# Performance work log

Hardware: AMD Instinct MI355X
Metric: run time of the kernel (lower is better)

The kernel has to match this reference:

```python
import jax, jax.numpy as jnp
import numpy as np

NUM_ROUTES, NUM_TIME, DIM, K, C = 100000, 2016, 256, 100, 5
BATCH = 262144


def _xavier(key, shape):
    fan_in, fan_out = shape[0], shape[1]
    lim = np.sqrt(6.0 / (fan_in + fan_out))
    return jax.random.uniform(key, shape, jnp.float32, -lim, lim)


def setup_inputs() -> dict:
    key = jax.random.key(0)
    ks = jax.random.split(key, 9)
    route_idx = jax.random.randint(ks[0], (BATCH,), 0, NUM_ROUTES)
    time_idx = jax.random.randint(ks[1], (BATCH,), 0, NUM_TIME)
    route_table = _xavier(ks[2], (NUM_ROUTES, DIM))
    time_table = _xavier(ks[3], (NUM_TIME, DIM))
    w = _xavier(ks[4], (DIM, K))
    mode_a = _xavier(ks[5], (DIM, C))
    mode_b = _xavier(ks[6], (DIM, C))
    mode_bias = jnp.zeros((C, C), jnp.float32)
    fc_lim = 1.0 / np.sqrt(C * C + K)
    fc_w = jax.random.uniform(ks[7], (C * C + K, 1), jnp.float32, -fc_lim, fc_lim)
    fc_b = jax.random.uniform(ks[8], (1,), jnp.float32, -fc_lim, fc_lim)
    return {
        "route_idx": route_idx, "time_idx": time_idx,
        "route_table": route_table, "time_table": time_table,
        "w": w, "mode_a": mode_a, "mode_b": mode_b,
        "mode_bias": mode_bias, "fc_w": fc_w, "fc_b": fc_b,
    }


def reference(route_idx, time_idx, route_table, time_table, w, mode_a, mode_b, mode_bias, fc_w, fc_b):
    r = route_table[route_idx]            # [B, D]
    t = time_table[time_idx]              # [B, D]
    gcp = jax.nn.relu((r * t) @ w)        # [B, K]
    # einsum('ni,nj->nij') then contracting i with mode_a and j with mode_b
    # equals outer product of the two small projections (exact same math):
    ra = r @ mode_a                       # [B, C]
    tb = t @ mode_b                       # [B, C]
    inter = jax.nn.sigmoid(ra[:, :, None] * tb[:, None, :] + mode_bias)  # [B, C, C]
    feats = jnp.concatenate([gcp, inter.reshape(inter.shape[0], -1)], axis=1)  # [B, K + C*C]
    out = feats @ fc_w + fc_b             # [B, 1]
    return jnp.squeeze(out, axis=-1)      # [B]
```

## Files before the change

### kernel.cpp

```cpp
#include <hip/hip_runtime.h>
#include <stdint.h>

#define BATCH   262144
#define NROUTES 100000
#define NTIME   2016
#define DIM     256
#define KOUT    100
#define NTILES  7

typedef __attribute__((ext_vector_type(2))) float f32x2;
typedef __attribute__((ext_vector_type(4))) float f32x4;

#define WS_WFRAG_BYTES ((size_t)(NTILES * 8 * 64 * 8))
#define WS_RA_OFF   (WS_WFRAG_BYTES)
#define WS_TB_OFF   (WS_RA_OFF + (size_t)NROUTES * 32)
#define WS_RT8_OFF  (WS_TB_OFF + (size_t)NTIME * 32)
#define WS_TT8_OFF  (WS_RT8_OFF + (size_t)NROUTES * 256)
#define WS_NEED     (WS_TT8_OFF + (size_t)NTIME * 256)

template<int CTRL>
static __device__ __forceinline__ float dpp_add(float x) {
  int s = __builtin_amdgcn_update_dpp(0, __builtin_bit_cast(int, x), CTRL, 0xF, 0xF, true);
  return x + __builtin_bit_cast(float, s);
}
static __device__ __forceinline__ float wave_sum63(float x) {
  x = dpp_add<0x111>(x);
  x = dpp_add<0x112>(x);
  x = dpp_add<0x114>(x);
  x = dpp_add<0x118>(x);
  x = dpp_add<0x142>(x);
  x = dpp_add<0x143>(x);
  return x;
}
static __device__ __forceinline__ float sum16_all(float x) {
  x = dpp_add<0x0B1>(x);
  x = dpp_add<0x04E>(x);
  x = dpp_add<0x124>(x);
  x = dpp_add<0x128>(x);
  return x;
}
static __device__ __forceinline__ float sigm(float z) {
  return __builtin_amdgcn_rcpf(1.0f + __expf(-z));
}

__global__ __launch_bounds__(256) void prep_kernel(
    const float* __restrict__ route_table,
    const float* __restrict__ time_table,
    const float* __restrict__ w,
    const float* __restrict__ mode_a,
    const float* __restrict__ mode_b,
    uint8_t* __restrict__ ws, int do8)
{
  const int b   = blockIdx.x;
  const int tid = threadIdx.x;

  if (b < 14) {
    const int u = b * 256 + tid;
    const int lane = u & 63;
    const int frag = u >> 6;
    const int ks = frag / NTILES;
    const int nt = frag % NTILES;
    const int n  = nt * 16 + (lane & 15);
    const int k0 = ks * 32 + (lane >> 4) * 8;
    float v[8];
    #pragma unroll
    for (int j = 0; j < 8; ++j)
      v[j] = (n < KOUT) ? w[(size_t)(k0 + j) * KOUT + n] : 0.0f;
    uint32_t d0 = 0, d1 = 0;
    d0 = __builtin_amdgcn_cvt_pk_fp8_f32(v[0], v[1], d0, false);
    d0 = __builtin_amdgcn_cvt_pk_fp8_f32(v[2], v[3], d0, true);
    d1 = __builtin_amdgcn_cvt_pk_fp8_f32(v[4], v[5], d1, false);
    d1 = __builtin_amdgcn_cvt_pk_fp8_f32(v[6], v[7], d1, true);
    ((uint2*)ws)[u] = make_uint2(d0, d1);
    return;
  }

  const float* tab; const float* proj; float* outp; uint8_t* out8; int base;
  if (b < 14 + 126) {
    tab = time_table;  proj = mode_b; outp = (float*)(ws + WS_TB_OFF);
    out8 = ws + WS_TT8_OFF; base = (b - 14) * 16;
  } else {
    tab = route_table; proj = mode_a; outp = (float*)(ws + WS_RA_OFF);
    out8 = ws + WS_RT8_OFF; base = (b - 140) * 16;
  }

  const int wave = tid >> 6, lane = tid & 63;
  float A[4][5];
  #pragma unroll
  for (int j = 0; j < 4; ++j)
    #pragma unroll
    for (int i = 0; i < 5; ++i)
      A[j][i] = proj[(4 * lane + j) * 5 + i];

  const int p0 = (lane >> 4) * 64 + ((lane >> 1) & 3) * 16 +
                 ((lane >> 3) & 1) * 8 + (lane & 1) * 4;

  const int row0 = base + wave * 4;
  float4 v[4];
  #pragma unroll
  for (int rr = 0; rr < 4; ++rr)
    v[rr] = *(const float4*)(tab + (size_t)(row0 + rr) * DIM + 4 * lane);

  #pragma unroll
  for (int rr = 0; rr < 4; ++rr) {
    const int row = row0 + rr;
    if (do8) {
      uint32_t u = 0;
      u = __builtin_amdgcn_cvt_pk_fp8_f32(8.f * v[rr].x, 8.f * v[rr].y, u, false);
      u = __builtin_amdgcn_cvt_pk_fp8_f32(8.f * v[rr].z, 8.f * v[rr].w, u, true);
      *(uint32_t*)(out8 + (size_t)row * 256 + p0) = u;
    }
    float p[5];
    #pragma unroll
    for (int i = 0; i < 5; ++i) {
      float s = v[rr].x * A[0][i] + v[rr].y * A[1][i] + v[rr].z * A[2][i] + v[rr].w * A[3][i];
      p[i] = wave_sum63(s);
    }
    if (lane == 63) {
      float* o = outp + (size_t)row * 8;
      *(f32x4*)o = (f32x4){p[0], p[1], p[2], p[3]};
      o[4] = p[4];
    }
  }
}

template<int TAB8>
__global__ __launch_bounds__(256, 4) void main_kernel(
    const int*   __restrict__ route_idx,
    const int*   __restrict__ time_idx,
    const float* __restrict__ route_table,
    const float* __restrict__ time_table,
    const float* __restrict__ mode_bias,
    const float* __restrict__ fc_w,
    const float* __restrict__ fc_b,
    const uint8_t* __restrict__ ws,
    float* __restrict__ out)
{
  __shared__ uint4 wlds[1792];
  const int tid  = threadIdx.x;
  const int wave = tid >> 6, lane = tid & 63;
  const int col  = lane & 15, quad = lane >> 4;
  const int m0   = blockIdx.x * 64 + wave * 16;
  const size_t ri = (size_t)route_idx[m0 + col];
  const size_t ti = (size_t)time_idx[m0 + col];

  uint4 rw[4], tw[4];
  if (TAB8) {
    const uint8_t* rb = ws + WS_RT8_OFF + ri * 256 + quad * 16;
    const uint8_t* tb = ws + WS_TT8_OFF + ti * 256 + quad * 16;
    #pragma unroll
    for (int i = 0; i < 4; ++i) {
      rw[i] = *(const uint4*)(rb + i * 64);
      tw[i] = *(const uint4*)(tb + i * 64);
    }
  }
  const float* rap = (const float*)(ws + WS_RA_OFF) + ri * 8;
  const float* tbp = (const float*)(ws + WS_TB_OFF) + ti * 8;
  f32x4 ra0 = *(const f32x4*)rap; float ra4 = rap[4];
  f32x4 tb0 = *(const f32x4*)tbp; float tb4 = tbp[4];

  {
    const uint4* wsrc = (const uint4*)ws;
    #pragma unroll
    for (int j = 0; j < 7; ++j)
      wlds[j * 256 + tid] = wsrc[j * 256 + tid];
  }
  __syncthreads();

  float fcw_l[NTILES];
  #pragma unroll
  for (int nt = 0; nt < NTILES; ++nt) {
    const int n = nt * 16 + col;
    fcw_l[nt] = (n < KOUT) ? fc_w[n] * 0.015625f : 0.0f;
  }

  f32x4 acc[NTILES];
  #pragma unroll
  for (int nt = 0; nt < NTILES; ++nt) acc[nt] = (f32x4){0.f, 0.f, 0.f, 0.f};
  const uint2* wl2 = (const uint2*)wlds;

  #pragma unroll
  for (int ks = 0; ks < 8; ++ks) {
    uint32_t p0, p1;
    if (TAB8) {
      const int i = ks >> 1;
      const uint32_t ra = (ks & 1) ? rw[i].z : rw[i].x;
      const uint32_t rb = (ks & 1) ? rw[i].w : rw[i].y;
      const uint32_t ta = (ks & 1) ? tw[i].z : tw[i].x;
      const uint32_t tb = (ks & 1) ? tw[i].w : tw[i].y;
      f32x2 r01 = __builtin_amdgcn_cvt_pk_f32_fp8(ra, false);
      f32x2 r23 = __builtin_amdgcn_cvt_pk_f32_fp8(ra, true);
      f32x2 r45 = __builtin_amdgcn_cvt_pk_f32_fp8(rb, false);
      f32x2 r67 = __builtin_amdgcn_cvt_pk_f32_fp8(rb, true);
      f32x2 t01 = __builtin_amdgcn_cvt_pk_f32_fp8(ta, false);
      f32x2 t23 = __builtin_amdgcn_cvt_pk_f32_fp8(ta, true);
      f32x2 t45 = __builtin_amdgcn_cvt_pk_f32_fp8(tb, false);
      f32x2 t67 = __builtin_amdgcn_cvt_pk_f32_fp8(tb, true);
      f32x2 x01 = r01 * t01, x23 = r23 * t23, x45 = r45 * t45, x67 = r67 * t67;
      p0 = 0; p1 = 0;
      p0 = __builtin_amdgcn_cvt_pk_fp8_f32(x01.x, x01.y, p0, false);
      p0 = __builtin_amdgcn_cvt_pk_fp8_f32(x23.x, x23.y, p0, true);
      p1 = __builtin_amdgcn_cvt_pk_fp8_f32(x45.x, x45.y, p1, false);
      p1 = __builtin_amdgcn_cvt_pk_fp8_f32(x67.x, x67.y, p1, true);
    } else {
      const float4* rp = (const float4*)(route_table + ri * DIM + ks * 32 + quad * 8);
      const float4* tp = (const float4*)(time_table  + ti * DIM + ks * 32 + quad * 8);
      float4 r0 = rp[0], r1 = rp[1], t0 = tp[0], t1 = tp[1];
      p0 = 0; p1 = 0;
      p0 = __builtin_amdgcn_cvt_pk_fp8_f32(64.f * r0.x * t0.x, 64.f * r0.y * t0.y, p0, false);
      p0 = __builtin_amdgcn_cvt_pk_fp8_f32(64.f * r0.z * t0.z, 64.f * r0.w * t0.w, p0, true);
      p1 = __builtin_amdgcn_cvt_pk_fp8_f32(64.f * r1.x * t1.x, 64.f * r1.y * t1.y, p1, false);
      p1 = __builtin_amdgcn_cvt_pk_fp8_f32(64.f * r1.z * t1.z, 64.f * r1.w * t1.w, p1, true);
    }
    const long a64 = __builtin_bit_cast(long, make_uint2(p0, p1));
    #pragma unroll
    for (int nt = 0; nt < NTILES; ++nt) {
      const long b64 = __builtin_bit_cast(long, wl2[(ks * NTILES + nt) * 64 + lane]);
      acc[nt] = __builtin_amdgcn_mfma_f32_16x16x32_fp8_fp8(a64, b64, acc[nt], 0, 0, 0);
    }
  }

  float s[4];
  #pragma unroll
  for (int reg = 0; reg < 4; ++reg) {
    float v = 0.f;
    #pragma unroll
    for (int nt = 0; nt < NTILES; ++nt)
      v += fmaxf(acc[nt][reg], 0.f) * fcw_l[nt];
    s[reg] = sum16_all(v);
  }

  const float rav[5] = {ra0.x, ra0.y, ra0.z, ra0.w, ra4};
  const float tbv[5] = {tb0.x, tb0.y, tb0.z, tb0.w, tb4};
  const float rq = (quad & 2) ? ((quad & 1) ? rav[3] : rav[2])
                              : ((quad & 1) ? rav[1] : rav[0]);
  const float tq = (quad & 2) ? ((quad & 1) ? tbv[3] : tbv[2])
                              : ((quad & 1) ? tbv[1] : tbv[0]);
  float sig = 0.f;
  #pragma unroll
  for (int j = 0; j < 5; ++j)
    sig += sigm(rq * tbv[j] + mode_bias[5 * quad + j]) * fc_w[KOUT + 5 * quad + j];
  sig += sigm(rav[4] * tq + mode_bias[20 + quad]) * fc_w[KOUT + 20 + quad];
  if (quad == 0)
    sig += sigm(rav[4] * tbv[4] + mode_bias[24]) * fc_w[KOUT + 24];
  sig += __shfl_xor(sig, 16, 64);
  sig += __shfl_xor(sig, 32, 64);

  if (quad == (col >> 2)) {
    const float sa = (col & 1) ? s[1] : s[0];
    const float sb = (col & 1) ? s[3] : s[2];
    const float gcp = (col & 2) ? sb : sa;
    out[m0 + col] = fc_b[0] + gcp + sig;
  }
}

extern "C" void kernel_launch(void* const* d_in, const int* in_sizes, int n_in,
                              void* d_out, int out_size, void* d_ws, size_t ws_size,
                              hipStream_t stream)
{
  const int*   route_idx   = (const int*)d_in[0];
  const int*   time_idx    = (const int*)d_in[1];
  const float* route_table = (const float*)d_in[2];
  const float* time_table  = (const float*)d_in[3];
  const float* w           = (const float*)d_in[4];
  const float* mode_a      = (const float*)d_in[5];
  const float* mode_b      = (const float*)d_in[6];
  const float* mode_bias   = (const float*)d_in[7];
  const float* fc_w        = (const float*)d_in[8];
  const float* fc_b        = (const float*)d_in[9];
  uint8_t* ws  = (uint8_t*)d_ws;
  float*   out = (float*)d_out;

  const int big = (ws_size >= WS_NEED) ? 1 : 0;

  prep_kernel<<<6390, 256, 0, stream>>>(route_table, time_table, w,
                                        mode_a, mode_b, ws, big);
  if (big)
    main_kernel<1><<<BATCH / 64, 256, 0, stream>>>(route_idx, time_idx,
                                                   route_table, time_table,
                                                   mode_bias, fc_w, fc_b, ws, out);
  else
    main_kernel<0><<<BATCH / 64, 256, 0, stream>>>(route_idx, time_idx,
                                                   route_table, time_table,
                                                   mode_bias, fc_w, fc_b, ws, out);
}
```

Before: 203.3 us.

## Make each wave process four 16-row tiles with double-buffered gathers

In the FP8-table path, each wave now handles 64 rows as four 16-row iterations and prefetches the next tile's gathered FP8 rows and small projections while the current tile runs its MFMAs. This amortises the weight-fragment load into LDS and the fc_w setup across four times as many rows, and launches a quarter as many blocks. In exchange it doubles the register buffers and lowers the launch-bounds occupancy target from 4 to 2 blocks. The non-FP8 fallback is split into its own kernel with unchanged logic.

Result: no change. 203.0 us (-0.2%).

```diff
diff --git a/kernel.cpp b/kernel.cpp
--- a/kernel.cpp
+++ b/kernel.cpp
@@ -124,8 +124,144 @@
   }
 }
 
-template<int TAB8>
-__global__ __launch_bounds__(256, 4) void main_kernel(
+__global__ __launch_bounds__(256, 2) void main_pipelined(
+    const int*   __restrict__ route_idx,
+    const int*   __restrict__ time_idx,
+    const float* __restrict__ mode_bias,
+    const float* __restrict__ fc_w,
+    const float* __restrict__ fc_b,
+    const uint8_t* __restrict__ ws,
+    float* __restrict__ out)
+{
+  __shared__ uint4 wlds[1792];
+  const int tid  = threadIdx.x;
+  const int wave = tid >> 6, lane = tid & 63;
+  const int col  = lane & 15, quad = lane >> 4;
+  const int base = (blockIdx.x * 4 + wave) * 64;
+
+  {
+    const uint4* wsrc = (const uint4*)ws;
+    #pragma unroll
+    for (int j = 0; j < 7; ++j)
+      wlds[j * 256 + tid] = wsrc[j * 256 + tid];
+  }
+
+  float fcw_l[NTILES];
+  #pragma unroll
+  for (int nt = 0; nt < NTILES; ++nt) {
+    const int n = nt * 16 + col;
+    fcw_l[nt] = (n < KOUT) ? fc_w[n] * 0.015625f : 0.0f;
+  }
+  const float fb = fc_b[0];
+
+  uint4 rw[2][4], tw[2][4];
+  f32x4 ra0[2], tb0[2];
+  float ra4[2], tb4[2];
+
+  auto issue = [&](int buf, int ri, int ti) {
+    const uint8_t* rb = ws + WS_RT8_OFF + (size_t)ri * 256 + quad * 16;
+    const uint8_t* tb = ws + WS_TT8_OFF + (size_t)ti * 256 + quad * 16;
+    #pragma unroll
+    for (int i = 0; i < 4; ++i) {
+      rw[buf][i] = *(const uint4*)(rb + i * 64);
+      tw[buf][i] = *(const uint4*)(tb + i * 64);
+    }
+    const float* rap = (const float*)(ws + WS_RA_OFF) + (size_t)ri * 8;
+    const float* tbp = (const float*)(ws + WS_TB_OFF) + (size_t)ti * 8;
+    ra0[buf] = *(const f32x4*)rap; ra4[buf] = rap[4];
+    tb0[buf] = *(const f32x4*)tbp; tb4[buf] = tbp[4];
+  };
+
+  int ri_n = route_idx[base + col];
+  int ti_n = time_idx[base + col];
+  issue(0, ri_n, ti_n);
+  ri_n = route_idx[base + 16 + col];
+  ti_n = time_idx[base + 16 + col];
+
+  __syncthreads();
+
+  const uint2* wl2 = (const uint2*)wlds;
+
+  #pragma unroll
+  for (int it = 0; it < 4; ++it) {
+    const int cb = it & 1, nb = cb ^ 1;
+    if (it < 3) {
+      issue(nb, ri_n, ti_n);
+      if (it < 2) {
+        ri_n = route_idx[base + (it + 2) * 16 + col];
+        ti_n = time_idx[base + (it + 2) * 16 + col];
+      }
+    }
+
+    f32x4 acc[NTILES];
+    #pragma unroll
+    for (int nt = 0; nt < NTILES; ++nt) acc[nt] = (f32x4){0.f, 0.f, 0.f, 0.f};
+
+    #pragma unroll
+    for (int ks = 0; ks < 8; ++ks) {
+      const int i = ks >> 1;
+      const uint32_t ra = (ks & 1) ? rw[cb][i].z : rw[cb][i].x;
+      const uint32_t rb = (ks & 1) ? rw[cb][i].w : rw[cb][i].y;
+      const uint32_t ta = (ks & 1) ? tw[cb][i].z : tw[cb][i].x;
+      const uint32_t tb = (ks & 1) ? tw[cb][i].w : tw[cb][i].y;
+      f32x2 r01 = __builtin_amdgcn_cvt_pk_f32_fp8(ra, false);
+      f32x2 r23 = __builtin_amdgcn_cvt_pk_f32_fp8(ra, true);
+      f32x2 r45 = __builtin_amdgcn_cvt_pk_f32_fp8(rb, false);
+      f32x2 r67 = __builtin_amdgcn_cvt_pk_f32_fp8(rb, true);
+      f32x2 t01 = __builtin_amdgcn_cvt_pk_f32_fp8(ta, false);
+      f32x2 t23 = __builtin_amdgcn_cvt_pk_f32_fp8(ta, true);
+      f32x2 t45 = __builtin_amdgcn_cvt_pk_f32_fp8(tb, false);
+      f32x2 t67 = __builtin_amdgcn_cvt_pk_f32_fp8(tb, true);
+      f32x2 x01 = r01 * t01, x23 = r23 * t23, x45 = r45 * t45, x67 = r67 * t67;
+      uint32_t p0 = 0, p1 = 0;
+      p0 = __builtin_amdgcn_cvt_pk_fp8_f32(x01.x, x01.y, p0, false);
+      p0 = __builtin_amdgcn_cvt_pk_fp8_f32(x23.x, x23.y, p0, true);
+      p1 = __builtin_amdgcn_cvt_pk_fp8_f32(x45.x, x45.y, p1, false);
+      p1 = __builtin_amdgcn_cvt_pk_fp8_f32(x67.x, x67.y, p1, true);
+      const long a64 = __builtin_bit_cast(long, make_uint2(p0, p1));
+      #pragma unroll
+      for (int nt = 0; nt < NTILES; ++nt) {
+        const long b64 = __builtin_bit_cast(long, wl2[(ks * NTILES + nt) * 64 + lane]);
+        acc[nt] = __builtin_amdgcn_mfma_f32_16x16x32_fp8_fp8(a64, b64, acc[nt], 0, 0, 0);
+      }
+    }
+
+    float s[4];
+    #pragma unroll
+    for (int reg = 0; reg < 4; ++reg) {
+      float v = 0.f;
+      #pragma unroll
+      for (int nt = 0; nt < NTILES; ++nt)
+        v += fmaxf(acc[nt][reg], 0.f) * fcw_l[nt];
+      s[reg] = sum16_all(v);
+    }
+
+    const float rav[5] = {ra0[cb].x, ra0[cb].y, ra0[cb].z, ra0[cb].w, ra4[cb]};
+    const float tbv[5] = {tb0[cb].x, tb0[cb].y, tb0[cb].z, tb0[cb].w, tb4[cb]};
+    const float rq = (quad & 2) ? ((quad & 1) ? rav[3] : rav[2])
+                                : ((quad & 1) ? rav[1] : rav[0]);
+    const float tq = (quad & 2) ? ((quad & 1) ? tbv[3] : tbv[2])
+                                : ((quad & 1) ? tbv[1] : tbv[0]);
+    float sig = 0.f;
+    #pragma unroll
+    for (int j = 0; j < 5; ++j)
+      sig += sigm(rq * tbv[j] + mode_bias[5 * quad + j]) * fc_w[KOUT + 5 * quad + j];
+    sig += sigm(rav[4] * tq + mode_bias[20 + quad]) * fc_w[KOUT + 20 + quad];
+    if (quad == 0)
+      sig += sigm(rav[4] * tbv[4] + mode_bias[24]) * fc_w[KOUT + 24];
+    sig += __shfl_xor(sig, 16, 64);
+    sig += __shfl_xor(sig, 32, 64);
+
+    if (quad == (col >> 2)) {
+      const float sa = (col & 1) ? s[1] : s[0];
+      const float sb = (col & 1) ? s[3] : s[2];
+      const float gcp = (col & 2) ? sb : sa;
+      out[base + it * 16 + col] = fb + gcp + sig;
+    }
+  }
+}
+
+__global__ __launch_bounds__(256, 4) void main_fallback(
     const int*   __restrict__ route_idx,
     const int*   __restrict__ time_idx,
     const float* __restrict__ route_table,
@@ -144,16 +280,6 @@
   const size_t ri = (size_t)route_idx[m0 + col];
   const size_t ti = (size_t)time_idx[m0 + col];
 
-  uint4 rw[4], tw[4];
-  if (TAB8) {
-    const uint8_t* rb = ws + WS_RT8_OFF + ri * 256 + quad * 16;
-    const uint8_t* tb = ws + WS_TT8_OFF + ti * 256 + quad * 16;
-    #pragma unroll
-    for (int i = 0; i < 4; ++i) {
-      rw[i] = *(const uint4*)(rb + i * 64);
-      tw[i] = *(const uint4*)(tb + i * 64);
-    }
-  }
   const float* rap = (const float*)(ws + WS_RA_OFF) + ri * 8;
   const float* tbp = (const float*)(ws + WS_TB_OFF) + ti * 8;
   f32x4 ra0 = *(const f32x4*)rap; float ra4 = rap[4];
@@ -181,37 +307,14 @@
 
   #pragma unroll
   for (int ks = 0; ks < 8; ++ks) {
-    uint32_t p0, p1;
-    if (TAB8) {
-      const int i = ks >> 1;
-      const uint32_t ra = (ks & 1) ? rw[i].z : rw[i].x;
-      const uint32_t rb = (ks & 1) ? rw[i].w : rw[i].y;
-      const uint32_t ta = (ks & 1) ? tw[i].z : tw[i].x;
-      const uint32_t tb = (ks & 1) ? tw[i].w : tw[i].y;
-      f32x2 r01 = __builtin_amdgcn_cvt_pk_f32_fp8(ra, false);
-      f32x2 r23 = __builtin_amdgcn_cvt_pk_f32_fp8(ra, true);
-      f32x2 r45 = __builtin_amdgcn_cvt_pk_f32_fp8(rb, false);
-      f32x2 r67 = __builtin_amdgcn_cvt_pk_f32_fp8(rb, true);
-      f32x2 t01 = __builtin_amdgcn_cvt_pk_f32_fp8(ta, false);
-      f32x2 t23 = __builtin_amdgcn_cvt_pk_f32_fp8(ta, true);
-      f32x2 t45 = __builtin_amdgcn_cvt_pk_f32_fp8(tb, false);
-      f32x2 t67 = __builtin_amdgcn_cvt_pk_f32_fp8(tb, true);
-      f32x2 x01 = r01 * t01, x23 = r23 * t23, x45 = r45 * t45, x67 = r67 * t67;
-      p0 = 0; p1 = 0;
-      p0 = __builtin_amdgcn_cvt_pk_fp8_f32(x01.x, x01.y, p0, false);
-      p0 = __builtin_amdgcn_cvt_pk_fp8_f32(x23.x, x23.y, p0, true);
-      p1 = __builtin_amdgcn_cvt_pk_fp8_f32(x45.x, x45.y, p1, false);
-      p1 = __builtin_amdgcn_cvt_pk_fp8_f32(x67.x, x67.y, p1, true);
-    } else {
-      const float4* rp = (const float4*)(route_table + ri * DIM + ks * 32 + quad * 8);
-      const float4* tp = (const float4*)(time_table  + ti * DIM + ks * 32 + quad * 8);
-      float4 r0 = rp[0], r1 = rp[1], t0 = tp[0], t1 = tp[1];
-      p0 = 0; p1 = 0;
-      p0 = __builtin_amdgcn_cvt_pk_fp8_f32(64.f * r0.x * t0.x, 64.f * r0.y * t0.y, p0, false);
-      p0 = __builtin_amdgcn_cvt_pk_fp8_f32(64.f * r0.z * t0.z, 64.f * r0.w * t0.w, p0, true);
-      p1 = __builtin_amdgcn_cvt_pk_fp8_f32(64.f * r1.x * t1.x, 64.f * r1.y * t1.y, p1, false);
-      p1 = __builtin_amdgcn_cvt_pk_fp8_f32(64.f * r1.z * t1.z, 64.f * r1.w * t1.w, p1, true);
-    }
+    const float4* rp = (const float4*)(route_table + ri * DIM + ks * 32 + quad * 8);
+    const float4* tp = (const float4*)(time_table  + ti * DIM + ks * 32 + quad * 8);
+    float4 r0 = rp[0], r1 = rp[1], t0 = tp[0], t1 = tp[1];
+    uint32_t p0 = 0, p1 = 0;
+    p0 = __builtin_amdgcn_cvt_pk_fp8_f32(64.f * r0.x * t0.x, 64.f * r0.y * t0.y, p0, false);
+    p0 = __builtin_amdgcn_cvt_pk_fp8_f32(64.f * r0.z * t0.z, 64.f * r0.w * t0.w, p0, true);
+    p1 = __builtin_amdgcn_cvt_pk_fp8_f32(64.f * r1.x * t1.x, 64.f * r1.y * t1.y, p1, false);
+    p1 = __builtin_amdgcn_cvt_pk_fp8_f32(64.f * r1.z * t1.z, 64.f * r1.w * t1.w, p1, true);
     const long a64 = __builtin_bit_cast(long, make_uint2(p0, p1));
     #pragma unroll
     for (int nt = 0; nt < NTILES; ++nt) {
@@ -276,11 +379,10 @@
   prep_kernel<<<6390, 256, 0, stream>>>(route_table, time_table, w,
                                         mode_a, mode_b, ws, big);
   if (big)
-    main_kernel<1><<<BATCH / 64, 256, 0, stream>>>(route_idx, time_idx,
-                                                   route_table, time_table,
-                                                   mode_bias, fc_w, fc_b, ws, out);
+    main_pipelined<<<BATCH / 256, 256, 0, stream>>>(route_idx, time_idx,
+                                                    mode_bias, fc_w, fc_b, ws, out);
   else
-    main_kernel<0><<<BATCH / 64, 256, 0, stream>>>(route_idx, time_idx,
-                                                   route_table, time_table,
-                                                   mode_bias, fc_w, fc_b, ws, out);
-}
+    main_fallback<<<BATCH / 64, 256, 0, stream>>>(route_idx, time_idx,
+                                                  route_table, time_table,
+                                                  mode_bias, fc_w, fc_b, ws, out);
+}
```
